# Kernel tuning notes

Hardware: AMD Instinct MI355X
Metric: run time of the kernel (lower is better)

The kernel has to match this reference:

```python
import jax, jax.numpy as jnp
import numpy as np

GRID_SIZE = 16
SPLINE_ORDER = 4
GRID_LO, GRID_HI = -1.0, 1.0
NUM_GRID = 2 * SPLINE_ORDER + GRID_SIZE + 1  # 25 knots
NUM_COEFFS = GRID_SIZE + SPLINE_ORDER        # 20 basis functions
B, IN_F, OUT_F = 2048, 512, 512


def _make_grid():
    h = (GRID_HI - GRID_LO) / GRID_SIZE
    t1 = -SPLINE_ORDER * h + GRID_LO
    t2 = (GRID_SIZE + SPLINE_ORDER + 1) * h + GRID_LO
    return jnp.linspace(t1, t2, NUM_GRID)


def _bspline_basis(x, grid):
    # x: [..., in]; returns [..., in, NUM_COEFFS] via De Boor recursion
    xe = x[..., None]
    bases = ((xe >= grid[:-1]) & (xe < grid[1:])).astype(x.dtype)
    for k in range(1, SPLINE_ORDER + 1):
        left = (xe - grid[:-k - 1]) / (grid[k:-1] - grid[:-k - 1]) * bases[..., :-1]
        right = (grid[k + 1:] - xe) / (grid[k + 1:] - grid[1:-k]) * bases[..., 1:]
        bases = left + right
    return bases


def setup_inputs() -> dict:
    key = jax.random.key(0)
    ks = jax.random.split(key, 5)
    fan = np.sqrt(1.0 / IN_F)
    return {
        "x": jax.random.normal(ks[0], (B, IN_F), jnp.float32),
        "prelu_weight": jax.random.normal(ks[1], (OUT_F, IN_F), jnp.float32) * 0.25,
        "base_weight": jax.random.uniform(ks[2], (OUT_F, IN_F), jnp.float32, -fan, fan),
        "spline_weight": jax.random.uniform(ks[3], (OUT_F, IN_F), jnp.float32, -fan, fan),
        "spline_coeffs": jax.random.normal(ks[4], (OUT_F, IN_F, NUM_COEFFS), jnp.float32) * 0.1,
    }


def reference(x, prelu_weight, base_weight, spline_weight, spline_coeffs):
    grid = _make_grid()
    xc = jnp.clip(x, GRID_LO, GRID_HI)
    pos = jax.nn.relu(xc)
    neg = xc - pos
    # base path: sum_j base_w[i,j]*(prelu_w[i,j]*neg[b,j] + pos[b,j])
    # fused: never materialize the [out, B, in] prelu output
    base = neg @ (base_weight * prelu_weight).T + pos @ base_weight.T  # [B, out]
    basis = _bspline_basis(xc, grid)  # [B, in, K]
    # spline path: fold spline_weight into coeffs, single contraction over (j,k)
    eff_coeffs = spline_weight[:, :, None] * spline_coeffs  # [out, in, K]
    spline = jnp.einsum('bjk,ijk->bi', basis, eff_coeffs)   # [B, out]
    return base + spline
```

## Files before the change

kernel.cpp:

```cpp
#include <hip/hip_runtime.h>


typedef _Float16 half_t;
typedef __attribute__((ext_vector_type(8))) _Float16 half8;
typedef __attribute__((ext_vector_type(4))) float floatx4;

#define B_DIM   2048
#define J_DIM   512
#define O_DIM   512
#define SLOTS   22
#define K_TOT   (J_DIM * SLOTS)
#define MTILE   128
#define NTILE   128
#define BK      32
#define KSPLIT  11
#define KS_LEN  (K_TOT / KSPLIT)
#define KCH     (KS_LEN / BK)
#define ZERO_BLKS 64

__device__ __forceinline__ void bspline5(float xc, int& k0, float Nv[5]) {
    const float invS = 7.68f;
    float u = (xc + 1.5f) * invS;
    int m = (int)u;
    m = min(max(m, 3), 19);
    k0 = m - 4;
    Nv[0] = 1.f; Nv[1] = 0.f; Nv[2] = 0.f; Nv[3] = 0.f; Nv[4] = 0.f;
#pragma unroll
    for (int d = 1; d <= 4; ++d) {
        float nw[5];
        float inv_d = 1.0f / (float)d;
#pragma unroll
        for (int r = 0; r < 5; ++r) {
            if (r > d) { nw[r] = 0.f; continue; }
            float kk = (float)(m - d + r);
            float acc = 0.f;
            if (r >= 1) acc += (u - kk) * Nv[r - 1];
            if (r < d)  acc += (kk + (float)(d + 1) - u) * Nv[r];
            nw[r] = acc * inv_d;
        }
#pragma unroll
        for (int r = 0; r < 5; ++r) Nv[r] = nw[r];
    }
}

__global__ __launch_bounds__(256) void prep_all(const float* __restrict__ x,
                                                const float* __restrict__ pw,
                                                const float* __restrict__ bw,
                                                const float* __restrict__ sw,
                                                const float* __restrict__ sc,
                                                half_t* __restrict__ A,
                                                half_t* __restrict__ Ct,
                                                float* __restrict__ out) {
    __shared__ half_t rec[J_DIM * SLOTS];
    int bid = blockIdx.x;
    int t = threadIdx.x;

    if (bid < ZERO_BLKS) {
        float4* o = (float4*)out;
        int base = bid * 4096;
#pragma unroll
        for (int i = 0; i < 16; ++i)
            o[base + i * 256 + t] = make_float4(0.f, 0.f, 0.f, 0.f);
        return;
    }

    if (bid < ZERO_BLKS + O_DIM) {
        int i = bid - ZERO_BLKS;
#pragma unroll
        for (int jj = 0; jj < 2; ++jj) {
            int j = t + jj * 256;
            size_t ij = (size_t)i * J_DIM + j;
            float s = sw[ij], b = bw[ij], p = pw[ij];
            const float4* scp4 = (const float4*)(sc + ij * 20);
            half_t* r = rec + j * SLOTS;
#pragma unroll
            for (int v = 0; v < 5; ++v) {
                float4 c4 = scp4[v];
                r[v * 4 + 0] = (half_t)(s * c4.x);
                r[v * 4 + 1] = (half_t)(s * c4.y);
                r[v * 4 + 2] = (half_t)(s * c4.z);
                r[v * 4 + 3] = (half_t)(s * c4.w);
            }
            r[20] = (half_t)(b * p);
            r[21] = (half_t)b;
        }
        __syncthreads();
        const uint4* src = (const uint4*)rec;
        uint4* dst = (uint4*)(Ct + (size_t)i * K_TOT);
        for (int idx = t; idx < (J_DIM * SLOTS * 2) / 16; idx += 256) dst[idx] = src[idx];
        return;
    }

    int b = bid - ZERO_BLKS - O_DIM;
#pragma unroll
    for (int jj = 0; jj < 2; ++jj) {
        int j = t + jj * 256;
        float xv = x[(size_t)b * J_DIM + j];
        float xc = fminf(fmaxf(xv, -1.f), 1.f);
        float pos = fmaxf(xc, 0.f);
        float neg = xc - pos;
        int k0; float Nv[5];
        bspline5(xc, k0, Nv);
        half_t* r = rec + j * SLOTS;
#pragma unroll
        for (int k = 0; k < 20; ++k) r[k] = (half_t)0.f;
#pragma unroll
        for (int rr = 0; rr < 5; ++rr) {
            int k = k0 + rr;
            if (k >= 0) r[k] = (half_t)Nv[rr];
        }
        r[20] = (half_t)neg;
        r[21] = (half_t)pos;
    }
    __syncthreads();
    const uint4* src = (const uint4*)rec;
    uint4* dst = (uint4*)(A + (size_t)b * K_TOT);
    for (int i = t; i < (J_DIM * SLOTS * 2) / 16; i += 256) dst[i] = src[i];
}

__global__ __launch_bounds__(256, 4) void gemm_f16(const half_t* __restrict__ A,
                                                   const half_t* __restrict__ Bt,
                                                   float* __restrict__ out) {
    __shared__ half_t As[2][MTILE * BK];
    __shared__ half_t Bs[2][NTILE * BK];

    int m0 = blockIdx.x * MTILE;
    int n0 = blockIdx.y * NTILE;
    int ks = blockIdx.z * KS_LEN;

    int t = threadIdx.x;
    int w = t >> 6;
    int l = t & 63;
    int wm = w >> 1, wn = w & 1;

    floatx4 acc[4][4] = {};

    int lrow = l >> 2;
    int lkof = (((l & 3) ^ ((l >> 3) & 3)) * 8);

    const half_t* gA = A + (size_t)m0 * K_TOT + ks;
    const half_t* gB = Bt + (size_t)n0 * K_TOT + ks;

    int q = l >> 4;
    int fr = l & 15;
    int qs = (q ^ ((fr >> 1) & 3)) * 8;

#define ISSUE_LOADS(c, p)                                                     \
    {                                                                         \
        int kb = (c) * BK;                                                    \
        _Pragma("unroll")                                                     \
        for (int n = 0; n < 2; ++n) {                                         \
            int r = (w * 2 + n) * 16 + lrow;                                  \
            __builtin_amdgcn_global_load_lds(                                 \
                (const __attribute__((address_space(1))) unsigned int*)       \
                    (gA + (size_t)r * K_TOT + kb + lkof),                     \
                (__attribute__((address_space(3))) unsigned int*)             \
                    (&As[p][0] + (w * 2 + n) * 512),                          \
                16, 0, 0);                                                    \
            __builtin_amdgcn_global_load_lds(                                 \
                (const __attribute__((address_space(1))) unsigned int*)       \
                    (gB + (size_t)r * K_TOT + kb + lkof),                     \
                (__attribute__((address_space(3))) unsigned int*)             \
                    (&Bs[p][0] + (w * 2 + n) * 512),                          \
                16, 0, 0);                                                    \
        }                                                                     \
    }

    ISSUE_LOADS(0, 0)
    int p = 0;
    for (int c = 0; c < KCH; ++c) {
        __syncthreads();
        if (c + 1 < KCH) ISSUE_LOADS(c + 1, p ^ 1)

        half8 af[4], bf[4];
#pragma unroll
        for (int mt = 0; mt < 4; ++mt)
            af[mt] = *(const half8*)(&As[p][0] + (wm * 64 + mt * 16 + fr) * BK + qs);
#pragma unroll
        for (int nt = 0; nt < 4; ++nt)
            bf[nt] = *(const half8*)(&Bs[p][0] + (wn * 64 + nt * 16 + fr) * BK + qs);
#pragma unroll
        for (int mt = 0; mt < 4; ++mt)
#pragma unroll
            for (int nt = 0; nt < 4; ++nt)
                acc[mt][nt] = __builtin_amdgcn_mfma_f32_16x16x32_f16(
                    af[mt], bf[nt], acc[mt][nt], 0, 0, 0);
        p ^= 1;
    }
#undef ISSUE_LOADS

#pragma unroll
    for (int mt = 0; mt < 4; ++mt)
#pragma unroll
        for (int nt = 0; nt < 4; ++nt) {
            int rr = m0 + wm * 64 + mt * 16 + q * 4;
            int cc = n0 + wn * 64 + nt * 16 + fr;
#pragma unroll
            for (int r = 0; r < 4; ++r)
                atomicAdd(out + (size_t)(rr + r) * O_DIM + cc, acc[mt][nt][r]);
        }
}

__global__ __launch_bounds__(256) void kan_fallback(const float* __restrict__ x,
                                                    const float* __restrict__ pw,
                                                    const float* __restrict__ bw,
                                                    const float* __restrict__ sw,
                                                    const float* __restrict__ sc,
                                                    float* __restrict__ out) {
    __shared__ float s_neg[J_DIM], s_pos[J_DIM], s_bas[J_DIM][5];
    __shared__ int s_k0[J_DIM];
    int b = blockIdx.x;
    int t = threadIdx.x;
#pragma unroll
    for (int jj = 0; jj < 2; ++jj) {
        int j = t + jj * 256;
        float xv = x[(size_t)b * J_DIM + j];
        float xc = fminf(fmaxf(xv, -1.f), 1.f);
        float pos = fmaxf(xc, 0.f);
        s_pos[j] = pos;
        s_neg[j] = xc - pos;
        int k0; float Nv[5];
        bspline5(xc, k0, Nv);
        s_k0[j] = k0;
#pragma unroll
        for (int r = 0; r < 5; ++r) s_bas[j][r] = Nv[r];
    }
    __syncthreads();
    for (int i = t; i < O_DIM; i += 256) {
        float acc = 0.f;
        for (int j = 0; j < J_DIM; ++j) {
            size_t ij = (size_t)i * J_DIM + j;
            float bwv = bw[ij];
            acc += bwv * (pw[ij] * s_neg[j] + s_pos[j]);
            int k0 = s_k0[j];
            const float* cp = sc + ij * 20;
            float sp = 0.f;
#pragma unroll
            for (int r = 0; r < 5; ++r) {
                int k = k0 + r;
                if (k >= 0) sp += s_bas[j][r] * cp[k];
            }
            acc += sw[ij] * sp;
        }
        out[(size_t)b * O_DIM + i] = acc;
    }
}

extern "C" void kernel_launch(void* const* d_in, const int* in_sizes, int n_in,
                              void* d_out, int out_size, void* d_ws, size_t ws_size,
                              hipStream_t stream) {
    const float* x  = (const float*)d_in[0];
    const float* pw = (const float*)d_in[1];
    const float* bw = (const float*)d_in[2];
    const float* sw = (const float*)d_in[3];
    const float* sc = (const float*)d_in[4];
    float* out = (float*)d_out;

    const size_t ws_needed = (size_t)(B_DIM + O_DIM) * K_TOT * sizeof(half_t);
    if (ws_size < ws_needed) {
        kan_fallback<<<B_DIM, 256, 0, stream>>>(x, pw, bw, sw, sc, out);
        return;
    }

    half_t* A  = (half_t*)d_ws;
    half_t* Ct = A + (size_t)B_DIM * K_TOT;

    prep_all<<<ZERO_BLKS + O_DIM + B_DIM, 256, 0, stream>>>(x, pw, bw, sw, sc, A, Ct, out);
    dim3 g(B_DIM / MTILE, O_DIM / NTILE, KSPLIT);
    gemm_f16<<<g, 256, 0, stream>>>(A, Ct, out);
}
```

Baseline: 142.5 us.

## Triple-buffer GEMM loads and replace split-K atomics with partial-sum reduction

```diff
diff --git a/kernel.cpp b/kernel.cpp
--- a/kernel.cpp
+++ b/kernel.cpp
@@ -13,9 +13,8 @@
 #define MTILE   128
 #define NTILE   128
 #define BK      32
-#define KSPLIT  11
-#define KS_LEN  (K_TOT / KSPLIT)
-#define KCH     (KS_LEN / BK)
+#define KSPLIT_P 8
+#define KSPLIT_A 11
 #define ZERO_BLKS 64
 
 __device__ __forceinline__ void bspline5(float xc, int& k0, float Nv[5]) {
@@ -118,15 +117,21 @@
     for (int i = t; i < (J_DIM * SLOTS * 2) / 16; i += 256) dst[i] = src[i];
 }
 
-__global__ __launch_bounds__(256, 4) void gemm_f16(const half_t* __restrict__ A,
+template<int KSPLIT_T, int OUTMODE>
+__global__ __launch_bounds__(256, 3) void gemm_f16(const half_t* __restrict__ A,
                                                    const half_t* __restrict__ Bt,
                                                    float* __restrict__ out) {
-    __shared__ half_t As[2][MTILE * BK];
-    __shared__ half_t Bs[2][NTILE * BK];
+    constexpr int KS_LEN_T = K_TOT / KSPLIT_T;
+    constexpr int KCH_T = KS_LEN_T / BK;
+    static_assert(KS_LEN_T % BK == 0, "k-split must be BK-aligned");
+    static_assert(KCH_T >= 2, "pipeline needs >= 2 chunks");
+
+    __shared__ half_t As[3][MTILE * BK];
+    __shared__ half_t Bs[3][NTILE * BK];
 
     int m0 = blockIdx.x * MTILE;
     int n0 = blockIdx.y * NTILE;
-    int ks = blockIdx.z * KS_LEN;
+    int ks = blockIdx.z * KS_LEN_T;
 
     int t = threadIdx.x;
     int w = t >> 6;
@@ -167,38 +172,82 @@
     }
 
     ISSUE_LOADS(0, 0)
-    int p = 0;
-    for (int c = 0; c < KCH; ++c) {
-        __syncthreads();
-        if (c + 1 < KCH) ISSUE_LOADS(c + 1, p ^ 1)
+    ISSUE_LOADS(1, 1)
+
+    int pb = 0;
+    for (int c = 0; c < KCH_T; ++c) {
+        if (c + 2 < KCH_T) {
+            asm volatile("s_waitcnt vmcnt(4)" ::: "memory");
+            __builtin_amdgcn_s_barrier();
+            int pn = pb + 2; if (pn >= 3) pn -= 3;
+            ISSUE_LOADS(c + 2, pn)
+        } else if (c + 2 == KCH_T) {
+            asm volatile("s_waitcnt vmcnt(4)" ::: "memory");
+            __builtin_amdgcn_s_barrier();
+        } else {
+            asm volatile("s_waitcnt vmcnt(0)" ::: "memory");
+            __builtin_amdgcn_s_barrier();
+        }
 
         half8 af[4], bf[4];
 #pragma unroll
         for (int mt = 0; mt < 4; ++mt)
-            af[mt] = *(const half8*)(&As[p][0] + (wm * 64 + mt * 16 + fr) * BK + qs);
+            af[mt] = *(const half8*)(&As[pb][0] + (wm * 64 + mt * 16 + fr) * BK + qs);
 #pragma unroll
         for (int nt = 0; nt < 4; ++nt)
-            bf[nt] = *(const half8*)(&Bs[p][0] + (wn * 64 + nt * 16 + fr) * BK + qs);
+            bf[nt] = *(const half8*)(&Bs[pb][0] + (wn * 64 + nt * 16 + fr) * BK + qs);
+
+        __builtin_amdgcn_s_setprio(1);
 #pragma unroll
         for (int mt = 0; mt < 4; ++mt)
 #pragma unroll
             for (int nt = 0; nt < 4; ++nt)
                 acc[mt][nt] = __builtin_amdgcn_mfma_f32_16x16x32_f16(
                     af[mt], bf[nt], acc[mt][nt], 0, 0, 0);
-        p ^= 1;
+        __builtin_amdgcn_s_setprio(0);
+
+        if (++pb == 3) pb = 0;
     }
 #undef ISSUE_LOADS
 
-#pragma unroll
-    for (int mt = 0; mt < 4; ++mt)
-#pragma unroll
-        for (int nt = 0; nt < 4; ++nt) {
-            int rr = m0 + wm * 64 + mt * 16 + q * 4;
-            int cc = n0 + wn * 64 + nt * 16 + fr;
-#pragma unroll
-            for (int r = 0; r < 4; ++r)
-                atomicAdd(out + (size_t)(rr + r) * O_DIM + cc, acc[mt][nt][r]);
-        }
+    if (OUTMODE == 0) {
+        float* dst = out + (size_t)blockIdx.z * ((size_t)B_DIM * O_DIM);
+#pragma unroll
+        for (int mt = 0; mt < 4; ++mt)
+#pragma unroll
+            for (int nt = 0; nt < 4; ++nt) {
+                int rr = m0 + wm * 64 + mt * 16 + q * 4;
+                int cc = n0 + wn * 64 + nt * 16 + fr;
+#pragma unroll
+                for (int r = 0; r < 4; ++r)
+                    dst[(size_t)(rr + r) * O_DIM + cc] = acc[mt][nt][r];
+            }
+    } else {
+#pragma unroll
+        for (int mt = 0; mt < 4; ++mt)
+#pragma unroll
+            for (int nt = 0; nt < 4; ++nt) {
+                int rr = m0 + wm * 64 + mt * 16 + q * 4;
+                int cc = n0 + wn * 64 + nt * 16 + fr;
+#pragma unroll
+                for (int r = 0; r < 4; ++r)
+                    atomicAdd(out + (size_t)(rr + r) * O_DIM + cc, acc[mt][nt][r]);
+            }
+    }
+}
+
+__global__ __launch_bounds__(256) void reduce8(const float* __restrict__ parts,
+                                               float* __restrict__ out) {
+    constexpr int N4 = B_DIM * O_DIM / 4;
+    int i = blockIdx.x * 256 + threadIdx.x;
+    const float4* p = (const float4*)parts;
+    float4 a = p[i];
+#pragma unroll
+    for (int z = 1; z < KSPLIT_P; ++z) {
+        float4 b = p[(size_t)z * N4 + i];
+        a.x += b.x; a.y += b.y; a.z += b.z; a.w += b.w;
+    }
+    ((float4*)out)[i] = a;
 }
 
 __global__ __launch_bounds__(256) void kan_fallback(const float* __restrict__ x,
@@ -256,16 +305,26 @@
     const float* sc = (const float*)d_in[4];
     float* out = (float*)d_out;
 
-    const size_t ws_needed = (size_t)(B_DIM + O_DIM) * K_TOT * sizeof(half_t);
-    if (ws_size < ws_needed) {
+    const size_t abct = (size_t)(B_DIM + O_DIM) * K_TOT * sizeof(half_t);
+    const size_t parts_bytes = (size_t)KSPLIT_P * B_DIM * O_DIM * sizeof(float);
+
+    if (ws_size >= abct + parts_bytes) {
+        half_t* A  = (half_t*)d_ws;
+        half_t* Ct = A + (size_t)B_DIM * K_TOT;
+        float* parts = (float*)((char*)d_ws + abct);
+
+        prep_all<<<ZERO_BLKS + O_DIM + B_DIM, 256, 0, stream>>>(x, pw, bw, sw, sc, A, Ct, out);
+        dim3 g(B_DIM / MTILE, O_DIM / NTILE, KSPLIT_P);
+        gemm_f16<KSPLIT_P, 0><<<g, 256, 0, stream>>>(A, Ct, parts);
+        reduce8<<<(B_DIM * O_DIM / 4) / 256, 256, 0, stream>>>(parts, out);
+    } else if (ws_size >= abct) {
+        half_t* A  = (half_t*)d_ws;
+        half_t* Ct = A + (size_t)B_DIM * K_TOT;
+
+        prep_all<<<ZERO_BLKS + O_DIM + B_DIM, 256, 0, stream>>>(x, pw, bw, sw, sc, A, Ct, out);
+        dim3 g(B_DIM / MTILE, O_DIM / NTILE, KSPLIT_A);
+        gemm_f16<KSPLIT_A, 1><<<g, 256, 0, stream>>>(A, Ct, out);
+    } else {
         kan_fallback<<<B_DIM, 256, 0, stream>>>(x, pw, bw, sw, sc, out);
-        return;
-    }
-
-    half_t* A  = (half_t*)d_ws;
-    half_t* Ct = A + (size_t)B_DIM * K_TOT;
-
-    prep_all<<<ZERO_BLKS + O_DIM + B_DIM, 256, 0, stream>>>(x, pw, bw, sw, sc, A, Ct, out);
-    dim3 g(B_DIM / MTILE, O_DIM / NTILE, KSPLIT);
-    gemm_f16<<<g, 256, 0, stream>>>(A, Ct, out);
-}
+    }
+}
```

Result: faster. 128.0 us (-10.2%).

## Rewrite split-K GEMM with 256x128 tiles, triple-buffered LDS and partial-sum reduction

Applied to the files above, without the earlier changes.

```diff
diff --git a/kernel.cpp b/kernel.cpp
--- a/kernel.cpp
+++ b/kernel.cpp
@@ -10,13 +10,10 @@
 #define O_DIM   512
 #define SLOTS   22
 #define K_TOT   (J_DIM * SLOTS)
-#define MTILE   128
-#define NTILE   128
-#define BK      32
-#define KSPLIT  11
-#define KS_LEN  (K_TOT / KSPLIT)
-#define KCH     (KS_LEN / BK)
-#define ZERO_BLKS 64
+#define BM      256
+#define BN      128
+#define BK      64
+#define KSPLIT_P 8
 
 __device__ __forceinline__ void bspline5(float xc, int& k0, float Nv[5]) {
     const float invS = 7.68f;
@@ -49,23 +46,13 @@
                                                 const float* __restrict__ sw,
                                                 const float* __restrict__ sc,
                                                 half_t* __restrict__ A,
-                                                half_t* __restrict__ Ct,
-                                                float* __restrict__ out) {
+                                                half_t* __restrict__ Ct) {
     __shared__ half_t rec[J_DIM * SLOTS];
     int bid = blockIdx.x;
     int t = threadIdx.x;
 
-    if (bid < ZERO_BLKS) {
-        float4* o = (float4*)out;
-        int base = bid * 4096;
-#pragma unroll
-        for (int i = 0; i < 16; ++i)
-            o[base + i * 256 + t] = make_float4(0.f, 0.f, 0.f, 0.f);
-        return;
-    }
-
-    if (bid < ZERO_BLKS + O_DIM) {
-        int i = bid - ZERO_BLKS;
+    if (bid < O_DIM) {
+        int i = bid;
 #pragma unroll
         for (int jj = 0; jj < 2; ++jj) {
             int j = t + jj * 256;
@@ -91,7 +78,7 @@
         return;
     }
 
-    int b = bid - ZERO_BLKS - O_DIM;
+    int b = bid - O_DIM;
 #pragma unroll
     for (int jj = 0; jj < 2; ++jj) {
         int j = t + jj * 256;
@@ -118,87 +105,151 @@
     for (int i = t; i < (J_DIM * SLOTS * 2) / 16; i += 256) dst[i] = src[i];
 }
 
-__global__ __launch_bounds__(256, 4) void gemm_f16(const half_t* __restrict__ A,
-                                                   const half_t* __restrict__ Bt,
-                                                   float* __restrict__ out) {
-    __shared__ half_t As[2][MTILE * BK];
-    __shared__ half_t Bs[2][NTILE * BK];
-
-    int m0 = blockIdx.x * MTILE;
-    int n0 = blockIdx.y * NTILE;
-    int ks = blockIdx.z * KS_LEN;
+__global__ __launch_bounds__(512, 2) void gemm8_f16(const half_t* __restrict__ A,
+                                                    const half_t* __restrict__ Bt,
+                                                    float* __restrict__ out) {
+    constexpr int KS_LEN = K_TOT / KSPLIT_P;
+    constexpr int NSTEP = KS_LEN / BK;
+
+    __shared__ half_t As[3][BM * BK];
+    __shared__ half_t Bs[3][BN * BK];
+
+    int lid = blockIdx.x + 8 * (blockIdx.y + 4 * blockIdx.z);
+    int bz = lid & 7;
+    int rem = lid >> 3;
+    int bx = rem & 7;
+    int by = rem >> 3;
+
+    int m0 = bx * BM, n0 = by * BN, ks = bz * KS_LEN;
 
     int t = threadIdx.x;
-    int w = t >> 6;
-    int l = t & 63;
-    int wm = w >> 1, wn = w & 1;
-
-    floatx4 acc[4][4] = {};
-
-    int lrow = l >> 2;
-    int lkof = (((l & 3) ^ ((l >> 3) & 3)) * 8);
+    int w = t >> 6, l = t & 63;
+    int wm = w >> 2, wn = w & 3;
+    int q = l >> 4, fr = l & 15;
 
     const half_t* gA = A + (size_t)m0 * K_TOT + ks;
     const half_t* gB = Bt + (size_t)n0 * K_TOT + ks;
 
-    int q = l >> 4;
-    int fr = l & 15;
-    int qs = (q ^ ((fr >> 1) & 3)) * 8;
-
-#define ISSUE_LOADS(c, p)                                                     \
-    {                                                                         \
-        int kb = (c) * BK;                                                    \
-        _Pragma("unroll")                                                     \
-        for (int n = 0; n < 2; ++n) {                                         \
-            int r = (w * 2 + n) * 16 + lrow;                                  \
-            __builtin_amdgcn_global_load_lds(                                 \
-                (const __attribute__((address_space(1))) unsigned int*)       \
-                    (gA + (size_t)r * K_TOT + kb + lkof),                     \
-                (__attribute__((address_space(3))) unsigned int*)             \
-                    (&As[p][0] + (w * 2 + n) * 512),                          \
-                16, 0, 0);                                                    \
-            __builtin_amdgcn_global_load_lds(                                 \
-                (const __attribute__((address_space(1))) unsigned int*)       \
-                    (gB + (size_t)r * K_TOT + kb + lkof),                     \
-                (__attribute__((address_space(3))) unsigned int*)             \
-                    (&Bs[p][0] + (w * 2 + n) * 512),                          \
-                16, 0, 0);                                                    \
-        }                                                                     \
-    }
-
-    ISSUE_LOADS(0, 0)
-    int p = 0;
-    for (int c = 0; c < KCH; ++c) {
-        __syncthreads();
-        if (c + 1 < KCH) ISSUE_LOADS(c + 1, p ^ 1)
-
-        half8 af[4], bf[4];
-#pragma unroll
-        for (int mt = 0; mt < 4; ++mt)
-            af[mt] = *(const half8*)(&As[p][0] + (wm * 64 + mt * 16 + fr) * BK + qs);
-#pragma unroll
-        for (int nt = 0; nt < 4; ++nt)
-            bf[nt] = *(const half8*)(&Bs[p][0] + (wn * 64 + nt * 16 + fr) * BK + qs);
-#pragma unroll
-        for (int mt = 0; mt < 4; ++mt)
-#pragma unroll
-            for (int nt = 0; nt < 4; ++nt)
-                acc[mt][nt] = __builtin_amdgcn_mfma_f32_16x16x32_f16(
-                    af[mt], bf[nt], acc[mt][nt], 0, 0, 0);
-        p ^= 1;
-    }
-#undef ISSUE_LOADS
-
-#pragma unroll
-    for (int mt = 0; mt < 4; ++mt)
-#pragma unroll
-        for (int nt = 0; nt < 4; ++nt) {
-            int rr = m0 + wm * 64 + mt * 16 + q * 4;
-            int cc = n0 + wn * 64 + nt * 16 + fr;
+    int srow = l >> 3;
+    int sqsw = ((l & 7) ^ srow) * 8;
+
+    int fsw0 = ((q)     ^ (fr & 7)) * 8;
+    int fsw1 = ((4 + q) ^ (fr & 7)) * 8;
+
+    floatx4 acc[8][2] = {};
+
+#define STAGE_A(kb, p, s)                                                     \
+    __builtin_amdgcn_global_load_lds(                                         \
+        (const __attribute__((address_space(1))) unsigned int*)               \
+            (gA + (size_t)((s) * 64 + w * 8 + srow) * K_TOT + (kb) + sqsw),   \
+        (__attribute__((address_space(3))) unsigned int*)                     \
+            (&As[p][((s) * 64 + w * 8) * BK]),                                \
+        16, 0, 0);
+#define STAGE_B(kb, p, s)                                                     \
+    __builtin_amdgcn_global_load_lds(                                         \
+        (const __attribute__((address_space(1))) unsigned int*)               \
+            (gB + (size_t)((s) * 64 + w * 8 + srow) * K_TOT + (kb) + sqsw),   \
+        (__attribute__((address_space(3))) unsigned int*)                     \
+            (&Bs[p][((s) * 64 + w * 8) * BK]),                                \
+        16, 0, 0);
+
+    STAGE_A(0, 0, 0) STAGE_A(0, 0, 1) STAGE_A(0, 0, 2) STAGE_A(0, 0, 3)
+    STAGE_B(0, 0, 0) STAGE_B(0, 0, 1)
+    STAGE_A(BK, 1, 0) STAGE_A(BK, 1, 1) STAGE_A(BK, 1, 2) STAGE_A(BK, 1, 3)
+    STAGE_B(BK, 1, 0) STAGE_B(BK, 1, 1)
+
+#define AFRD(mt, kss) (*(const half8*)(Ab + ((wm << 7) + ((mt) << 4) + fr) * BK + (kss)))
+#define BFRD(nt, kss) (*(const half8*)(Bb + ((wn << 5) + ((nt) << 4) + fr) * BK + (kss)))
+#define MM(mt, a0, a1)                                                            \
+    acc[mt][0] = __builtin_amdgcn_mfma_f32_16x16x32_f16(a0, bfr00, acc[mt][0], 0, 0, 0); \
+    acc[mt][0] = __builtin_amdgcn_mfma_f32_16x16x32_f16(a1, bfr01, acc[mt][0], 0, 0, 0); \
+    acc[mt][1] = __builtin_amdgcn_mfma_f32_16x16x32_f16(a0, bfr10, acc[mt][1], 0, 0, 0); \
+    acc[mt][1] = __builtin_amdgcn_mfma_f32_16x16x32_f16(a1, bfr11, acc[mt][1], 0, 0, 0);
+
+    int cb = 0;
+    for (int T = 0; T < NSTEP; ++T) {
+        if (T < NSTEP - 1) { asm volatile("s_waitcnt vmcnt(6)" ::: "memory"); }
+        else               { asm volatile("s_waitcnt vmcnt(0)" ::: "memory"); }
+        __builtin_amdgcn_s_barrier();
+
+        const bool st = (T + 2 < NSTEP);
+        int sb = cb + 2; if (sb >= 3) sb -= 3;
+        const int kb = (T + 2) * BK;
+        const half_t* Ab = &As[cb][0];
+        const half_t* Bb = &Bs[cb][0];
+
+        half8 a0, a1, a2, a3;
+
+        half8 bfr00 = BFRD(0, fsw0), bfr01 = BFRD(0, fsw1);
+        half8 bfr10 = BFRD(1, fsw0), bfr11 = BFRD(1, fsw1);
+        a0 = AFRD(0, fsw0); a1 = AFRD(0, fsw1);
+        a2 = AFRD(1, fsw0); a3 = AFRD(1, fsw1);
+        if (st) { STAGE_A(kb, sb, 0) STAGE_A(kb, sb, 1) }
+        __builtin_amdgcn_s_barrier();
+        __builtin_amdgcn_s_setprio(1);
+        MM(0, a0, a1) MM(1, a2, a3)
+        __builtin_amdgcn_s_setprio(0);
+        __builtin_amdgcn_s_barrier();
+
+        a0 = AFRD(2, fsw0); a1 = AFRD(2, fsw1);
+        a2 = AFRD(3, fsw0); a3 = AFRD(3, fsw1);
+        if (st) { STAGE_A(kb, sb, 2) STAGE_A(kb, sb, 3) }
+        __builtin_amdgcn_s_barrier();
+        __builtin_amdgcn_s_setprio(1);
+        MM(2, a0, a1) MM(3, a2, a3)
+        __builtin_amdgcn_s_setprio(0);
+        __builtin_amdgcn_s_barrier();
+
+        a0 = AFRD(4, fsw0); a1 = AFRD(4, fsw1);
+        a2 = AFRD(5, fsw0); a3 = AFRD(5, fsw1);
+        if (st) { STAGE_B(kb, sb, 0) }
+        __builtin_amdgcn_s_barrier();
+        __builtin_amdgcn_s_setprio(1);
+        MM(4, a0, a1) MM(5, a2, a3)
+        __builtin_amdgcn_s_setprio(0);
+        __builtin_amdgcn_s_barrier();
+
+        a0 = AFRD(6, fsw0); a1 = AFRD(6, fsw1);
+        a2 = AFRD(7, fsw0); a3 = AFRD(7, fsw1);
+        if (st) { STAGE_B(kb, sb, 1) }
+        __builtin_amdgcn_s_barrier();
+        __builtin_amdgcn_s_setprio(1);
+        MM(6, a0, a1) MM(7, a2, a3)
+        __builtin_amdgcn_s_setprio(0);
+
+        if (++cb == 3) cb = 0;
+    }
+#undef MM
+#undef AFRD
+#undef BFRD
+#undef STAGE_A
+#undef STAGE_B
+
+    float* dst = out + (size_t)bz * ((size_t)B_DIM * O_DIM);
+#pragma unroll
+    for (int mt = 0; mt < 8; ++mt)
+#pragma unroll
+        for (int nt = 0; nt < 2; ++nt) {
+            int rr = m0 + wm * 128 + mt * 16 + q * 4;
+            int cc = n0 + wn * 32 + nt * 16 + fr;
 #pragma unroll
             for (int r = 0; r < 4; ++r)
-                atomicAdd(out + (size_t)(rr + r) * O_DIM + cc, acc[mt][nt][r]);
-        }
+                dst[(size_t)(rr + r) * O_DIM + cc] = acc[mt][nt][r];
+        }
+}
+
+__global__ __launch_bounds__(256) void reduce8(const float* __restrict__ parts,
+                                               float* __restrict__ out) {
+    constexpr int N4 = B_DIM * O_DIM / 4;
+    int i = blockIdx.x * 256 + threadIdx.x;
+    const float4* p = (const float4*)parts;
+    float4 a = p[i];
+#pragma unroll
+    for (int z = 1; z < KSPLIT_P; ++z) {
+        float4 b = p[(size_t)z * N4 + i];
+        a.x += b.x; a.y += b.y; a.z += b.z; a.w += b.w;
+    }
+    ((float4*)out)[i] = a;
 }
 
 __global__ __launch_bounds__(256) void kan_fallback(const float* __restrict__ x,
@@ -256,16 +307,19 @@
     const float* sc = (const float*)d_in[4];
     float* out = (float*)d_out;
 
-    const size_t ws_needed = (size_t)(B_DIM + O_DIM) * K_TOT * sizeof(half_t);
-    if (ws_size < ws_needed) {
+    const size_t abct = (size_t)(B_DIM + O_DIM) * K_TOT * sizeof(half_t);
+    const size_t parts_bytes = (size_t)KSPLIT_P * B_DIM * O_DIM * sizeof(float);
+
+    if (ws_size >= abct + parts_bytes) {
+        half_t* A  = (half_t*)d_ws;
+        half_t* Ct = A + (size_t)B_DIM * K_TOT;
+        float* parts = (float*)((char*)d_ws + abct);
+
+        prep_all<<<O_DIM + B_DIM, 256, 0, stream>>>(x, pw, bw, sw, sc, A, Ct);
+        dim3 g(B_DIM / BM, O_DIM / BN, KSPLIT_P);
+        gemm8_f16<<<g, 512, 0, stream>>>(A, Ct, parts);
+        reduce8<<<(B_DIM * O_DIM / 4) / 256, 256, 0, stream>>>(parts, out);
+    } else {
         kan_fallback<<<B_DIM, 256, 0, stream>>>(x, pw, bw, sw, sc, out);
-        return;
-    }
-
-    half_t* A  = (half_t*)d_ws;
-    half_t* Ct = A + (size_t)B_DIM * K_TOT;
-
-    prep_all<<<ZERO_BLKS + O_DIM + B_DIM, 256, 0, stream>>>(x, pw, bw, sw, sc, A, Ct, out);
-    dim3 g(B_DIM / MTILE, O_DIM / NTILE, KSPLIT);
-    gemm_f16<<<g, 256, 0, stream>>>(A, Ct, out);
-}
+    }
+}
```

New measurement: 128.0 us. 10.2% less time.
